# Optimization experiments

Hardware: AMD Instinct MI355X
Metric: run time of the kernel (lower is better)

The kernel has to match this reference:

```python
import jax, jax.numpy as jnp
import numpy as np

N = 50000      # nodes
E = 500000     # edges
R = 4          # num_relations
B = 512        # num graphs in batch
IN = 64        # in_embd
DIN = 6 * IN   # concat of 6 embeddings
H = 256        # layer_embd
O = 256        # out_embd
CARD = [33, 5, 3, 4, 2, 3]


def setup_inputs() -> dict:
    key = jax.random.key(0)
    ks = jax.random.split(key, 24)
    cols = [jax.random.randint(ks[i], (N,), 0, CARD[i], dtype=jnp.int32) for i in range(6)]
    x = jnp.stack(cols, axis=1)                                     # [N,6] categorical atom features
    edge_index = jax.random.randint(ks[6], (2, E), 0, N, dtype=jnp.int32)
    edge_type = jax.random.randint(ks[7], (E,), 0, R, dtype=jnp.int32)
    batch = jnp.sort(jax.random.randint(ks[8], (N,), 0, B, dtype=jnp.int32))

    def g(k, shape, scale):
        return jax.random.normal(k, shape, jnp.float32) * scale

    inp = dict(x=x, edge_index=edge_index, edge_type=edge_type, batch=batch)
    for i in range(6):
        inp[f"emb{i}"] = g(ks[9 + i], (CARD[i], IN), 1.0)
    inp["W1"] = g(ks[15], (R, DIN, H), 0.05)
    inp["root1"] = g(ks[16], (DIN, H), 0.05)
    inp["b1"] = jnp.zeros((H,), jnp.float32)
    inp["W2"] = g(ks[17], (R, H, O), 0.06)
    inp["root2"] = g(ks[18], (H, O), 0.06)
    inp["b2"] = jnp.zeros((O,), jnp.float32)
    inp["g1_w"] = g(ks[19], (O, O), 0.06)
    inp["g1_b"] = jnp.zeros((O,), jnp.float32)
    inp["bn_g"] = jnp.ones((O,), jnp.float32)
    inp["bn_b"] = jnp.zeros((O,), jnp.float32)
    inp["g2_w"] = g(ks[20], (O, 1), 0.06)
    inp["g2_b"] = jnp.zeros((1,), jnp.float32)
    inp["gl_w"] = g(ks[21], (O, 1), 0.06)
    inp["gl_b"] = jnp.zeros((1,), jnp.float32)
    return inp


def rgcn_conv(h, src, dst, etype, W, root, bias):
    # PyG RGCNConv: out_i = x_i @ root + bias + sum_r mean_{j in N_r(i)} (x_j @ W_r)
    xw = jnp.einsum('nd,rdo->rno', h, W)                 # [R,N,O] relation-transformed nodes
    msg = xw[etype, src]                                  # [E,O] gather per edge
    seg = dst * R + etype                                 # combined (node, relation) segment id
    sums = jax.ops.segment_sum(msg, seg, num_segments=N * R)
    cnt = jax.ops.segment_sum(jnp.ones((msg.shape[0],), h.dtype), seg, num_segments=N * R)
    mean = sums / jnp.maximum(cnt, 1.0)[:, None]          # per-relation mean aggregation
    agg = mean.reshape(N, R, -1).sum(axis=1)              # sum over relations
    return agg + h @ root + bias


def reference(x, edge_index, edge_type, batch,
              emb0, emb1, emb2, emb3, emb4, emb5,
              W1, root1, b1, W2, root2, b2,
              g1_w, g1_b, bn_g, bn_b, g2_w, g2_b, gl_w, gl_b):
    embs = [emb0, emb1, emb2, emb3, emb4, emb5]
    feats = jnp.concatenate([embs[i][x[:, i]] for i in range(6)], axis=1)  # [N, 6*IN]
    src, dst = edge_index[0], edge_index[1]
    h = jax.nn.sigmoid(rgcn_conv(feats, src, dst, edge_type, W1, root1, b1))
    h = jax.nn.sigmoid(rgcn_conv(h, src, dst, edge_type, W2, root2, b2))    # [N,O]

    # GlobalAttention gate_nn: Linear -> BatchNorm1d (training-mode stats) -> ReLU -> Linear
    g = h @ g1_w + g1_b
    mu = g.mean(axis=0)
    var = g.var(axis=0)                                   # biased var, as torch BN forward
    g = (g - mu) / jnp.sqrt(var + 1e-5) * bn_g + bn_b
    gate = jax.nn.relu(g) @ g2_w + g2_b                   # [N,1]

    # segment softmax over graphs
    gmax = jax.ops.segment_max(gate, batch, num_segments=B)
    e = jnp.exp(gate - gmax[batch])
    denom = jax.ops.segment_sum(e, batch, num_segments=B)
    attn = e / (denom[batch] + 1e-16)
    pooled = jax.ops.segment_sum(attn * h, batch, num_segments=B)  # [B,O]

    return jax.nn.sigmoid(pooled @ gl_w + gl_b)           # [B,1]
```

## Files before the change

### kernel.cpp

```cpp
#include <hip/hip_runtime.h>
#include <hip/hip_bf16.h>
#include <cstdint>

#define NN 50000
#define NE 500000
#define NR 4
#define NBATCH 512
#define HD 256
#define NSEG (NN*NR)
#define CHUNK 25000

__constant__ int c_off[6] = {0,33,38,41,45,47};

__device__ __forceinline__ float sigf(float x){ return 1.0f/(1.0f+__expf(-x)); }
__device__ __forceinline__ float bf2f(unsigned short b){ return __uint_as_float((unsigned)b<<16); }
__device__ __forceinline__ unsigned short f2bf(float f){
  unsigned u = __float_as_uint(f);
  return (unsigned short)((u + 0x7fffu + ((u>>16)&1u)) >> 16);
}

typedef short bf16raw8 __attribute__((ext_vector_type(8)));
typedef float f32x4v  __attribute__((ext_vector_type(4)));
union LD16 { uint4 u; bf16raw8 v; };

__global__ void k_weff(const float* __restrict__ e0,const float* __restrict__ e1,
                       const float* __restrict__ e2,const float* __restrict__ e3,
                       const float* __restrict__ e4,const float* __restrict__ e5,
                       const float* __restrict__ W, int rstride,
                       float* __restrict__ out){
  int rc = blockIdx.x, h = threadIdx.x;
  int r = rc/50, cg = rc%50;
  int j, cl;
  if      (cg>=47){j=5;cl=cg-47;} else if (cg>=45){j=4;cl=cg-45;}
  else if (cg>=41){j=3;cl=cg-41;} else if (cg>=38){j=2;cl=cg-38;}
  else if (cg>=33){j=1;cl=cg-33;} else            {j=0;cl=cg;}
  const float* emb = j==0?e0:j==1?e1:j==2?e2:j==3?e3:j==4?e4:e5;
  const float* wb = W + (size_t)r*rstride + (size_t)(j*64)*HD + h;
  float acc = 0.f;
  #pragma unroll 8
  for (int k=0;k<64;k++) acc += emb[cl*64+k]*wb[(size_t)k*HD];
  out[(size_t)rc*HD+h] = acc;
}

__global__ void k_cnt(const int* __restrict__ ei, const int* __restrict__ et,
                      int* __restrict__ cnt){
  int e = blockIdx.x*256 + threadIdx.x;
  if (e >= NE) return;
  atomicAdd(&cnt[ei[NE+e]*NR + et[e]], 1);
}

__global__ void k_b1t(const float* __restrict__ W1eff, const float* __restrict__ R1eff,
                      unsigned short* __restrict__ B1t){
  int id = blockIdx.x*256 + threadIdx.x;
  int k = id & 255, o = id >> 8;
  float v = 0.f;
  if (k < 200) v = W1eff[(size_t)k*HD + o];
  else if (k < 250) v = R1eff[(size_t)(k-200)*HD + o];
  B1t[(size_t)o*256 + k] = f2bf(v);
}

__global__ void k_tconv(const float* __restrict__ W, unsigned short* __restrict__ Wt,
                        int K, int O, int dstStride, int dstOff){
  int id = blockIdx.x*256 + threadIdx.x;
  if (id >= K*O) return;
  int k = id % K, o = id / K;
  Wt[(size_t)o*dstStride + dstOff + k] = f2bf(W[(size_t)k*O + o]);
}

#define SC_T 256
#define SC_NB ((NSEG/4 + SC_T - 1)/SC_T)

__global__ void k_scan1(const int* __restrict__ cnt, int* __restrict__ bsum){
  __shared__ int sh[SC_T];
  int b = blockIdx.x, t = threadIdx.x;
  int i4 = b*SC_T + t;
  int s = 0;
  if (i4 < NSEG/4){ int4 v = ((const int4*)cnt)[i4]; s = v.x+v.y+v.z+v.w; }
  sh[t] = s; __syncthreads();
  for (int o=128;o>0;o>>=1){ if (t<o) sh[t]+=sh[t+o]; __syncthreads(); }
  if (t==0) bsum[b] = sh[0];
}

__global__ void k_scan2(const int* __restrict__ bsum, int* __restrict__ boff,
                        int* __restrict__ offs){
  __shared__ int sh[256];
  int t = threadIdx.x;
  int v = (t < SC_NB) ? bsum[t] : 0;
  sh[t] = v; __syncthreads();
  for (int o=1;o<256;o<<=1){
    int add = (t>=o) ? sh[t-o] : 0; __syncthreads();
    sh[t] += add; __syncthreads();
  }
  if (t < SC_NB) boff[t] = sh[t] - v;
  if (t == 255) offs[NSEG] = sh[255];
}

__global__ void k_scan3(const int* __restrict__ cnt, const int* __restrict__ boff,
                        int* __restrict__ offs, int* __restrict__ cursor){
  __shared__ int sh[SC_T];
  int b = blockIdx.x, t = threadIdx.x;
  int i4 = b*SC_T + t;
  int4 v = {0,0,0,0};
  if (i4 < NSEG/4) v = ((const int4*)cnt)[i4];
  int s = v.x+v.y+v.z+v.w;
  sh[t] = s; __syncthreads();
  for (int o=1;o<256;o<<=1){
    int add = (t>=o) ? sh[t-o] : 0; __syncthreads();
    sh[t] += add; __syncthreads();
  }
  if (i4 < NSEG/4){
    int excl = sh[t] - s + boff[b];
    int4 ov; ov.x = excl; ov.y = ov.x+v.x; ov.z = ov.y+v.y; ov.w = ov.z+v.z;
    ((int4*)offs)[i4] = ov; ((int4*)cursor)[i4] = ov;
  }
}

__global__ void k_bin(const int* __restrict__ ei, const int* __restrict__ et,
                      int* __restrict__ cursor, int* __restrict__ esrc){
  int e = blockIdx.x*256 + threadIdx.x;
  if (e >= NE) return;
  int s = ei[e], d = ei[NE+e], t = et[e];
  int slot = atomicAdd(&cursor[d*NR + t], 1);
  esrc[slot] = s;
}

__global__ void k_buildseg(const int* __restrict__ x, const int* __restrict__ offs,
                           const int* __restrict__ esrc, unsigned short* __restrict__ A1){
  int n = blockIdx.x, t = threadIdx.x;
  float v = 0.f;
  if (t < 200){
    int r = t/50, bin = t%50;
    int j, cl;
    if      (bin>=47){j=5;cl=bin-47;} else if (bin>=45){j=4;cl=bin-45;}
    else if (bin>=41){j=3;cl=bin-41;} else if (bin>=38){j=2;cl=bin-38;}
    else if (bin>=33){j=1;cl=bin-33;} else            {j=0;cl=bin;}
    int a = offs[n*NR+r], e2 = offs[n*NR+r+1];
    int c = 0;
    for (int e=a;e<e2;e++){
      int s = esrc[e];
      c += (x[s*6+j] == cl) ? 1 : 0;
    }
    v = (float)c / (float)max(e2-a, 1);
  } else if (t < 250){
    int cg = t - 200;
    #pragma unroll
    for (int j=0;j<6;j++) if (cg == c_off[j] + x[n*6+j]) v = 1.f;
  }
  A1[(size_t)n*256 + t] = f2bf(v);
}

__global__ void k_agg(const int* __restrict__ offs, const int* __restrict__ esrc,
                      const unsigned short* __restrict__ h1, unsigned short* __restrict__ agg,
                      int base, int m){
  int gid = blockIdx.x*256 + threadIdx.x;
  int n = gid >> 6;
  if (n >= m) return;
  int lane = gid & 63;
  int gn = base + n;
  #pragma unroll
  for (int r=0;r<NR;r++){
    int a = offs[gn*NR+r], b = offs[gn*NR+r+1];
    float a0=0.f,a1=0.f,a2=0.f,a3=0.f;
    for (int e=a;e<b;e++){
      int s = esrc[e];
      ushort4 v = *(const ushort4*)(h1 + (size_t)s*HD + lane*4);
      a0+=bf2f(v.x); a1+=bf2f(v.y); a2+=bf2f(v.z); a3+=bf2f(v.w);
    }
    float iv = 1.0f / (float)max(b-a, 1);
    ushort4 o;
    o.x=f2bf(a0*iv); o.y=f2bf(a1*iv); o.z=f2bf(a2*iv); o.w=f2bf(a3*iv);
    *(ushort4*)(agg + (size_t)n*(NR*HD) + r*HD + lane*4) = o;
  }
}

template<int NK1, int NK2, bool SIG>
__global__ __launch_bounds__(512) void k_mfma(
    const unsigned short* __restrict__ A,  int lda,
    const unsigned short* __restrict__ A2, int lda2,
    const unsigned short* __restrict__ Bt,
    const float* __restrict__ bias,
    unsigned short* __restrict__ outB,
    int M){
  constexpr int NK = NK1 + NK2;
  constexpr int K  = NK * 32;
  int tid = threadIdx.x;
  int wave = tid >> 6, lane = tid & 63;
  int wm = (wave >> 1) * 32, wn = (wave & 1) * 64;
  int bm = blockIdx.y * 128, bn = blockIdx.x * 128;
  int lrow = lane & 15, lk8 = (lane >> 4) * 8;

  const unsigned short* aP[2];
  const unsigned short* a2P[2];
  const unsigned short* bP[4];
  #pragma unroll
  for (int mi=0;mi<2;mi++){
    int row = bm + wm + mi*16 + lrow; if (row > M-1) row = M-1;
    aP[mi]  = A  + (size_t)row*lda  + lk8;
    if (NK2 > 0) a2P[mi] = A2 + (size_t)row*lda2 + lk8;
  }
  #pragma unroll
  for (int nj=0;nj<4;nj++){
    int col = bn + wn + nj*16 + lrow;
    bP[nj] = Bt + (size_t)col*K + lk8;
  }

  f32x4v acc[2][4] = {};
  bf16raw8 aF[2][2], bF[2][4];

  #pragma unroll
  for (int mi=0;mi<2;mi++){ LD16 t; t.u = *(const uint4*)(aP[mi]); aF[0][mi]=t.v; }
  #pragma unroll
  for (int nj=0;nj<4;nj++){ LD16 t; t.u = *(const uint4*)(bP[nj]); bF[0][nj]=t.v; }

  #pragma unroll
  for (int k=0;k<NK;k++){
    int cur = k & 1, nxt = cur ^ 1;
    if (k+1 < NK){
      if (k+1 < NK1){
        #pragma unroll
        for (int mi=0;mi<2;mi++){ LD16 t; t.u = *(const uint4*)(aP[mi] + (k+1)*32); aF[nxt][mi]=t.v; }
      } else {
        #pragma unroll
        for (int mi=0;mi<2;mi++){ LD16 t; t.u = *(const uint4*)(a2P[mi] + (k+1-NK1)*32); aF[nxt][mi]=t.v; }
      }
      #pragma unroll
      for (int nj=0;nj<4;nj++){ LD16 t; t.u = *(const uint4*)(bP[nj] + (k+1)*32); bF[nxt][nj]=t.v; }
    }
    #pragma unroll
    for (int mi=0;mi<2;mi++)
      #pragma unroll
      for (int nj=0;nj<4;nj++)
        acc[mi][nj] = __builtin_amdgcn_mfma_f32_16x16x32_bf16(aF[cur][mi], bF[cur][nj], acc[mi][nj], 0, 0, 0);
  }

  int r0 = (lane >> 4) * 4;
  #pragma unroll
  for (int mi = 0; mi < 2; mi++){
    #pragma unroll
    for (int i = 0; i < 4; i++){
      int row = bm + wm + mi*16 + r0 + i;
      if (row >= M) continue;
      #pragma unroll
      for (int nj = 0; nj < 4; nj++){
        int col = bn + wn + nj*16 + lrow;
        float v = acc[mi][nj][i];
        if (bias) v += bias[col];
        if (SIG) v = sigf(v);
        outB[(size_t)row*HD + col] = f2bf(v);
      }
    }
  }
}

__global__ void k_bnstats(const unsigned short* __restrict__ g, float* __restrict__ chan){
  int c = threadIdx.x;
  int r0 = blockIdx.x*128;
  int rend = min(r0+128, NN);
  float s=0.f, q=0.f;
  for (int row=r0; row<rend; row++){
    float v = bf2f(g[(size_t)row*HD + c]);
    s += v; q += v*v;
  }
  atomicAdd(&chan[c], s); atomicAdd(&chan[HD+c], q);
}

__global__ void k_bnfin(const float* __restrict__ chan, const float* __restrict__ bng,
                        const float* __restrict__ bnb, float* __restrict__ bnp){
  int c = threadIdx.x;
  float mu = chan[c]/(float)NN;
  float var = chan[HD+c]/(float)NN - mu*mu;
  float scale = bng[c]*rsqrtf(var + 1e-5f);
  bnp[c] = bnb[c] - mu*scale;
  bnp[HD+c] = scale;
}

__global__ void k_gate(const unsigned short* __restrict__ g, const float* __restrict__ bnp,
                       const float* __restrict__ g2w, const float* __restrict__ g2b,
                       float* __restrict__ gate){
  int lane = threadIdx.x & 63;
  int n = blockIdx.x*4 + (threadIdx.x>>6);
  if (n >= NN) return;
  float s = 0.f;
  #pragma unroll
  for (int k=0;k<4;k++){
    int c = lane + k*64;
    float v = bf2f(g[(size_t)n*HD + c])*bnp[HD+c] + bnp[c];
    v = fmaxf(v, 0.f);
    s += v * g2w[c];
  }
  #pragma unroll
  for (int o=32;o>0;o>>=1) s += __shfl_down(s, o);
  if (lane==0) gate[n] = s + g2b[0];
}

__global__ void k_goffs(const int* __restrict__ batch, int* __restrict__ goffs){
  int n = blockIdx.x*256 + threadIdx.x;
  if (n >= NN) return;
  int b = batch[n];
  int prev = (n == 0) ? -1 : batch[n-1];
  for (int gg = prev+1; gg <= b; gg++) goffs[gg] = n;
  if (n == NN-1){ for (int gg = b+1; gg <= NBATCH; gg++) goffs[gg] = NN; }
}

__global__ __launch_bounds__(256) void k_poolg(
    const unsigned short* __restrict__ h2, const float* __restrict__ gate,
    const int* __restrict__ goffs, const float* __restrict__ glw,
    const float* __restrict__ glb, float* __restrict__ out){
  __shared__ float red[256];
  int b = blockIdx.x, tid = threadIdx.x;
  int a = goffs[b], e = goffs[b+1];

  float m = -3.4e38f;
  for (int n = a + tid; n < e; n += 256) m = fmaxf(m, gate[n]);
  red[tid] = m; __syncthreads();
  for (int o = 128; o > 0; o >>= 1){ if (tid < o) red[tid] = fmaxf(red[tid], red[tid+o]); __syncthreads(); }
  m = red[0]; __syncthreads();

  float s = 0.f;
  for (int n = a + tid; n < e; n += 256) s += __expf(gate[n] - m);
  red[tid] = s; __syncthreads();
  for (int o = 128; o > 0; o >>= 1){ if (tid < o) red[tid] += red[tid+o]; __syncthreads(); }
  float denom = red[0] + 1e-16f; __syncthreads();

  float acc = 0.f;
  #pragma unroll 4
  for (int n = a; n < e; n++){
    float ev = __expf(gate[n] - m);
    acc += ev * bf2f(h2[(size_t)n*HD + tid]);
  }
  acc /= denom;

  red[tid] = acc * glw[tid]; __syncthreads();
  for (int o = 128; o > 0; o >>= 1){ if (tid < o) red[tid] += red[tid+o]; __syncthreads(); }
  if (tid == 0) out[b] = sigf(red[0] + glb[0]);
}

extern "C" void kernel_launch(void* const* d_in, const int* in_sizes, int n_in,
                              void* d_out, int out_size, void* d_ws, size_t ws_size,
                              hipStream_t stream) {
  const int* x     = (const int*)d_in[0];
  const int* ei    = (const int*)d_in[1];
  const int* et    = (const int*)d_in[2];
  const int* batch = (const int*)d_in[3];
  const float* emb0 = (const float*)d_in[4];
  const float* emb1 = (const float*)d_in[5];
  const float* emb2 = (const float*)d_in[6];
  const float* emb3 = (const float*)d_in[7];
  const float* emb4 = (const float*)d_in[8];
  const float* emb5 = (const float*)d_in[9];
  const float* W1    = (const float*)d_in[10];
  const float* root1 = (const float*)d_in[11];
  const float* b1    = (const float*)d_in[12];
  const float* W2    = (const float*)d_in[13];
  const float* root2 = (const float*)d_in[14];
  const float* b2    = (const float*)d_in[15];
  const float* g1w   = (const float*)d_in[16];
  const float* g1b   = (const float*)d_in[17];
  const float* bng   = (const float*)d_in[18];
  const float* bnb   = (const float*)d_in[19];
  const float* g2w   = (const float*)d_in[20];
  const float* g2b   = (const float*)d_in[21];
  const float* glw   = (const float*)d_in[22];
  const float* glb   = (const float*)d_in[23];
  float* out = (float*)d_out;

  char* w = (char*)d_ws;
  auto alloc = [&](size_t bytes)->char* {
    char* p = w; w += (bytes + 255) & ~(size_t)255; return p;
  };
  char* gReg = alloc((size_t)NN*HD*2);
  unsigned short* A1 = (unsigned short*)gReg;
  unsigned short* g  = (unsigned short*)gReg;
  unsigned short* agg  = (unsigned short*)alloc((size_t)CHUNK*NR*HD*2);
  unsigned short* h1   = (unsigned short*)alloc((size_t)NN*HD*2);
  unsigned short* hRes = (unsigned short*)alloc((size_t)NN*HD*2);
  int*   cnt  = (int*)alloc((size_t)NSEG*sizeof(int));
  int*   offs = (int*)alloc((size_t)(NSEG+1)*sizeof(int));
  int*   cursor=(int*)alloc((size_t)NSEG*sizeof(int));
  int*   bsum = (int*)alloc((size_t)SC_NB*sizeof(int));
  int*   boff = (int*)alloc((size_t)SC_NB*sizeof(int));
  int*   esrc = (int*)alloc((size_t)NE*sizeof(int));
  float* W1eff= (float*)alloc((size_t)200*HD*sizeof(float));
  float* R1eff= (float*)alloc((size_t)50*HD*sizeof(float));
  unsigned short* B1t  = (unsigned short*)alloc((size_t)256*256*2);
  unsigned short* BtL2 = (unsigned short*)alloc((size_t)256*1280*2);
  unsigned short* g1wt = (unsigned short*)alloc((size_t)256*256*2);
  float* gate = (float*)alloc((size_t)NN*sizeof(float));
  int*   goffs= (int*)alloc((size_t)(NBATCH+1)*sizeof(int));
  float* chan = (float*)alloc((size_t)2*HD*sizeof(float));
  float* bnp  = (float*)alloc((size_t)2*HD*sizeof(float));

  hipMemsetAsync(cnt,  0, (size_t)NSEG*sizeof(int), stream);
  hipMemsetAsync(chan, 0, (size_t)2*HD*sizeof(float), stream);

  k_weff<<<NR*50, HD, 0, stream>>>(emb0,emb1,emb2,emb3,emb4,emb5, W1, 384*HD, W1eff);
  k_weff<<<50,    HD, 0, stream>>>(emb0,emb1,emb2,emb3,emb4,emb5, root1, 0, R1eff);
  k_b1t<<<256, 256, 0, stream>>>(W1eff, R1eff, B1t);
  k_tconv<<<256, 256, 0, stream>>>(root2, BtL2, 256, 256, 1280, 0);
  k_tconv<<<1024, 256, 0, stream>>>(W2, BtL2, 1024, 256, 1280, 256);
  k_tconv<<<256, 256, 0, stream>>>(g1w, g1wt, 256, 256, 256, 0);

  k_cnt<<<(NE+255)/256, 256, 0, stream>>>(ei, et, cnt);
  k_scan1<<<SC_NB, SC_T, 0, stream>>>(cnt, bsum);
  k_scan2<<<1, 256, 0, stream>>>(bsum, boff, offs);
  k_scan3<<<SC_NB, SC_T, 0, stream>>>(cnt, boff, offs, cursor);
  k_bin<<<(NE+255)/256, 256, 0, stream>>>(ei, et, cursor, esrc);

  k_buildseg<<<NN, 256, 0, stream>>>(x, offs, esrc, A1);

  k_goffs<<<(NN+255)/256, 256, 0, stream>>>(batch, goffs);

  dim3 gFull(2, (NN+127)/128);
  k_mfma<8,0,true><<<gFull, 512, 0, stream>>>(A1, 256, nullptr, 0, B1t, b1, h1, NN);

  for (int c0 = 0; c0 < NN; c0 += CHUNK){
    int m = min(CHUNK, NN - c0);
    k_agg<<<(m*64+255)/256, 256, 0, stream>>>(offs, esrc, h1, agg, c0, m);
    dim3 gC(2, (m+127)/128);
    k_mfma<8,32,true><<<gC, 512, 0, stream>>>(h1 + (size_t)c0*HD, 256, agg, NR*HD,
                                              BtL2, b2, hRes + (size_t)c0*HD, m);
  }

  k_mfma<8,0,false><<<gFull, 512, 0, stream>>>(hRes, 256, nullptr, 0, g1wt, g1b, g, NN);
  k_bnstats<<<(NN+127)/128, HD, 0, stream>>>(g, chan);
  k_bnfin<<<1, HD, 0, stream>>>(chan, bng, bnb, bnp);

  k_gate<<<(NN+3)/4, 256, 0, stream>>>(g, bnp, g2w, g2b, gate);
  k_poolg<<<NBATCH, 256, 0, stream>>>(hRes, gate, goffs, glw, glb, out);
}
```

Measured before the change: 704.5 us.

## Transform-then-aggregate for RGCN layer 2 instead of aggregate-then-GEMM

Layer 2 used to average raw neighbour features per relation into a large K=1280 operand and then run one GEMM. Now it first computes per-relation node transforms h1@W_r (two relations at a time) plus the root term with plain K=256 GEMMs into a z buffer. Two gather kernels then average the transformed rows per relation and finish with bias and sigmoid. This removes the big agg buffer and the chunked loop, at the cost of writing and gathering transformed rows, which adds bf16 rounding of the intermediate terms.

```diff
diff --git a/kernel.cpp b/kernel.cpp
--- a/kernel.cpp
+++ b/kernel.cpp
@@ -8,7 +8,6 @@
 #define NBATCH 512
 #define HD 256
 #define NSEG (NN*NR)
-#define CHUNK 25000
 
 __constant__ int c_off[6] = {0,33,38,41,45,47};
 
@@ -60,11 +59,11 @@
 }
 
 __global__ void k_tconv(const float* __restrict__ W, unsigned short* __restrict__ Wt,
-                        int K, int O, int dstStride, int dstOff){
+                        int K, int O){
   int id = blockIdx.x*256 + threadIdx.x;
   if (id >= K*O) return;
   int k = id % K, o = id / K;
-  Wt[(size_t)o*dstStride + dstOff + k] = f2bf(W[(size_t)k*O + o]);
+  Wt[(size_t)o*256 + k] = f2bf(W[(size_t)k*O + o]);
 }
 
 #define SC_T 256
@@ -149,40 +148,16 @@
   A1[(size_t)n*256 + t] = f2bf(v);
 }
 
-__global__ void k_agg(const int* __restrict__ offs, const int* __restrict__ esrc,
-                      const unsigned short* __restrict__ h1, unsigned short* __restrict__ agg,
-                      int base, int m){
-  int gid = blockIdx.x*256 + threadIdx.x;
-  int n = gid >> 6;
-  if (n >= m) return;
-  int lane = gid & 63;
-  int gn = base + n;
-  #pragma unroll
-  for (int r=0;r<NR;r++){
-    int a = offs[gn*NR+r], b = offs[gn*NR+r+1];
-    float a0=0.f,a1=0.f,a2=0.f,a3=0.f;
-    for (int e=a;e<b;e++){
-      int s = esrc[e];
-      ushort4 v = *(const ushort4*)(h1 + (size_t)s*HD + lane*4);
-      a0+=bf2f(v.x); a1+=bf2f(v.y); a2+=bf2f(v.z); a3+=bf2f(v.w);
-    }
-    float iv = 1.0f / (float)max(b-a, 1);
-    ushort4 o;
-    o.x=f2bf(a0*iv); o.y=f2bf(a1*iv); o.z=f2bf(a2*iv); o.w=f2bf(a3*iv);
-    *(ushort4*)(agg + (size_t)n*(NR*HD) + r*HD + lane*4) = o;
-  }
-}
-
-template<int NK1, int NK2, bool SIG>
+template<bool SIG>
 __global__ __launch_bounds__(512) void k_mfma(
     const unsigned short* __restrict__ A,  int lda,
-    const unsigned short* __restrict__ A2, int lda2,
     const unsigned short* __restrict__ Bt,
     const float* __restrict__ bias,
-    unsigned short* __restrict__ outB,
+    unsigned short* __restrict__ out0, int ldc0, int n0,
+    unsigned short* __restrict__ out1, int ldc1,
     int M){
-  constexpr int NK = NK1 + NK2;
-  constexpr int K  = NK * 32;
+  constexpr int NK = 8;
+  constexpr int K  = 256;
   int tid = threadIdx.x;
   int wave = tid >> 6, lane = tid & 63;
   int wm = (wave >> 1) * 32, wn = (wave & 1) * 64;
@@ -190,13 +165,11 @@
   int lrow = lane & 15, lk8 = (lane >> 4) * 8;
 
   const unsigned short* aP[2];
-  const unsigned short* a2P[2];
   const unsigned short* bP[4];
   #pragma unroll
   for (int mi=0;mi<2;mi++){
     int row = bm + wm + mi*16 + lrow; if (row > M-1) row = M-1;
-    aP[mi]  = A  + (size_t)row*lda  + lk8;
-    if (NK2 > 0) a2P[mi] = A2 + (size_t)row*lda2 + lk8;
+    aP[mi] = A + (size_t)row*lda + lk8;
   }
   #pragma unroll
   for (int nj=0;nj<4;nj++){
@@ -216,13 +189,8 @@
   for (int k=0;k<NK;k++){
     int cur = k & 1, nxt = cur ^ 1;
     if (k+1 < NK){
-      if (k+1 < NK1){
-        #pragma unroll
-        for (int mi=0;mi<2;mi++){ LD16 t; t.u = *(const uint4*)(aP[mi] + (k+1)*32); aF[nxt][mi]=t.v; }
-      } else {
-        #pragma unroll
-        for (int mi=0;mi<2;mi++){ LD16 t; t.u = *(const uint4*)(a2P[mi] + (k+1-NK1)*32); aF[nxt][mi]=t.v; }
-      }
+      #pragma unroll
+      for (int mi=0;mi<2;mi++){ LD16 t; t.u = *(const uint4*)(aP[mi] + (k+1)*32); aF[nxt][mi]=t.v; }
       #pragma unroll
       for (int nj=0;nj<4;nj++){ LD16 t; t.u = *(const uint4*)(bP[nj] + (k+1)*32); bF[nxt][nj]=t.v; }
     }
@@ -246,10 +214,69 @@
         float v = acc[mi][nj][i];
         if (bias) v += bias[col];
         if (SIG) v = sigf(v);
-        outB[(size_t)row*HD + col] = f2bf(v);
+        if (col < n0) out0[(size_t)row*ldc0 + col] = f2bf(v);
+        else          out1[(size_t)row*ldc1 + (col - n0)] = f2bf(v);
       }
     }
   }
+}
+
+__global__ void k_comb1(const int* __restrict__ offs, const int* __restrict__ esrc,
+                        const unsigned short* __restrict__ zbuf,
+                        unsigned short* __restrict__ pacc){
+  int gid = blockIdx.x*256 + threadIdx.x;
+  int n = gid >> 6;
+  if (n >= NN) return;
+  int lane = gid & 63;
+  float t0=0.f,t1=0.f,t2=0.f,t3=0.f;
+  #pragma unroll
+  for (int r=0;r<2;r++){
+    int a = offs[n*NR+r], b = offs[n*NR+r+1];
+    float a0=0.f,a1=0.f,a2=0.f,a3=0.f;
+    for (int e=a;e<b;e++){
+      int s = esrc[e];
+      ushort4 v = *(const ushort4*)(zbuf + (size_t)s*512 + r*256 + lane*4);
+      a0+=bf2f(v.x); a1+=bf2f(v.y); a2+=bf2f(v.z); a3+=bf2f(v.w);
+    }
+    float iv = 1.0f / (float)max(b-a, 1);
+    t0+=a0*iv; t1+=a1*iv; t2+=a2*iv; t3+=a3*iv;
+  }
+  ushort4 o; o.x=f2bf(t0); o.y=f2bf(t1); o.z=f2bf(t2); o.w=f2bf(t3);
+  *(ushort4*)(pacc + (size_t)n*HD + lane*4) = o;
+}
+
+__global__ void k_comb2(const int* __restrict__ offs, const int* __restrict__ esrc,
+                        const unsigned short* __restrict__ zbuf,
+                        const unsigned short* __restrict__ pacc,
+                        const unsigned short* __restrict__ rootbuf,
+                        const float* __restrict__ b2,
+                        unsigned short* __restrict__ h2){
+  int gid = blockIdx.x*256 + threadIdx.x;
+  int n = gid >> 6;
+  if (n >= NN) return;
+  int lane = gid & 63;
+  float t0=0.f,t1=0.f,t2=0.f,t3=0.f;
+  #pragma unroll
+  for (int r=0;r<2;r++){
+    int a = offs[n*NR+2+r], b = offs[n*NR+2+r+1];
+    float a0=0.f,a1=0.f,a2=0.f,a3=0.f;
+    for (int e=a;e<b;e++){
+      int s = esrc[e];
+      ushort4 v = *(const ushort4*)(zbuf + (size_t)s*512 + r*256 + lane*4);
+      a0+=bf2f(v.x); a1+=bf2f(v.y); a2+=bf2f(v.z); a3+=bf2f(v.w);
+    }
+    float iv = 1.0f / (float)max(b-a, 1);
+    t0+=a0*iv; t1+=a1*iv; t2+=a2*iv; t3+=a3*iv;
+  }
+  ushort4 p = *(const ushort4*)(pacc + (size_t)n*HD + lane*4);
+  ushort4 rt= *(const ushort4*)(rootbuf + (size_t)n*HD + lane*4);
+  float4 bb = *(const float4*)(b2 + lane*4);
+  ushort4 o;
+  o.x = f2bf(sigf(t0 + bf2f(p.x) + bf2f(rt.x) + bb.x));
+  o.y = f2bf(sigf(t1 + bf2f(p.y) + bf2f(rt.y) + bb.y));
+  o.z = f2bf(sigf(t2 + bf2f(p.z) + bf2f(rt.z) + bb.z));
+  o.w = f2bf(sigf(t3 + bf2f(p.w) + bf2f(rt.w) + bb.w));
+  *(ushort4*)(h2 + (size_t)n*HD + lane*4) = o;
 }
 
 __global__ void k_bnstats(const unsigned short* __restrict__ g, float* __restrict__ chan){
@@ -368,22 +395,25 @@
   auto alloc = [&](size_t bytes)->char* {
     char* p = w; w += (bytes + 255) & ~(size_t)255; return p;
   };
-  char* gReg = alloc((size_t)NN*HD*2);
-  unsigned short* A1 = (unsigned short*)gReg;
-  unsigned short* g  = (unsigned short*)gReg;
-  unsigned short* agg  = (unsigned short*)alloc((size_t)CHUNK*NR*HD*2);
-  unsigned short* h1   = (unsigned short*)alloc((size_t)NN*HD*2);
-  unsigned short* hRes = (unsigned short*)alloc((size_t)NN*HD*2);
+  char* slotA = alloc((size_t)NN*HD*2);
+  unsigned short* A1      = (unsigned short*)slotA;
+  unsigned short* rootbuf = (unsigned short*)slotA;
+  unsigned short* g       = (unsigned short*)slotA;
+  unsigned short* h1 = (unsigned short*)alloc((size_t)NN*HD*2);
+  unsigned short* h2 = h1;
+  unsigned short* zbuf = (unsigned short*)alloc((size_t)NN*512*2);
+  unsigned short* pacc = (unsigned short*)alloc((size_t)NN*HD*2);
   int*   cnt  = (int*)alloc((size_t)NSEG*sizeof(int));
+  int*   cursor = cnt;
   int*   offs = (int*)alloc((size_t)(NSEG+1)*sizeof(int));
-  int*   cursor=(int*)alloc((size_t)NSEG*sizeof(int));
   int*   bsum = (int*)alloc((size_t)SC_NB*sizeof(int));
   int*   boff = (int*)alloc((size_t)SC_NB*sizeof(int));
   int*   esrc = (int*)alloc((size_t)NE*sizeof(int));
   float* W1eff= (float*)alloc((size_t)200*HD*sizeof(float));
   float* R1eff= (float*)alloc((size_t)50*HD*sizeof(float));
   unsigned short* B1t  = (unsigned short*)alloc((size_t)256*256*2);
-  unsigned short* BtL2 = (unsigned short*)alloc((size_t)256*1280*2);
+  unsigned short* Btz1 = (unsigned short*)alloc((size_t)768*256*2);
+  unsigned short* Btz2 = (unsigned short*)alloc((size_t)512*256*2);
   unsigned short* g1wt = (unsigned short*)alloc((size_t)256*256*2);
   float* gate = (float*)alloc((size_t)NN*sizeof(float));
   int*   goffs= (int*)alloc((size_t)(NBATCH+1)*sizeof(int));
@@ -396,9 +426,12 @@
   k_weff<<<NR*50, HD, 0, stream>>>(emb0,emb1,emb2,emb3,emb4,emb5, W1, 384*HD, W1eff);
   k_weff<<<50,    HD, 0, stream>>>(emb0,emb1,emb2,emb3,emb4,emb5, root1, 0, R1eff);
   k_b1t<<<256, 256, 0, stream>>>(W1eff, R1eff, B1t);
-  k_tconv<<<256, 256, 0, stream>>>(root2, BtL2, 256, 256, 1280, 0);
-  k_tconv<<<1024, 256, 0, stream>>>(W2, BtL2, 1024, 256, 1280, 256);
-  k_tconv<<<256, 256, 0, stream>>>(g1w, g1wt, 256, 256, 256, 0);
+  k_tconv<<<256, 256, 0, stream>>>(W2,               Btz1,           256, 256);
+  k_tconv<<<256, 256, 0, stream>>>(W2 + 256*256,     Btz1 + 256*256, 256, 256);
+  k_tconv<<<256, 256, 0, stream>>>(root2,            Btz1 + 512*256, 256, 256);
+  k_tconv<<<256, 256, 0, stream>>>(W2 + 2*256*256,   Btz2,           256, 256);
+  k_tconv<<<256, 256, 0, stream>>>(W2 + 3*256*256,   Btz2 + 256*256, 256, 256);
+  k_tconv<<<256, 256, 0, stream>>>(g1w,              g1wt,           256, 256);
 
   k_cnt<<<(NE+255)/256, 256, 0, stream>>>(ei, et, cnt);
   k_scan1<<<SC_NB, SC_T, 0, stream>>>(cnt, bsum);
@@ -410,21 +443,21 @@
 
   k_goffs<<<(NN+255)/256, 256, 0, stream>>>(batch, goffs);
 
-  dim3 gFull(2, (NN+127)/128);
-  k_mfma<8,0,true><<<gFull, 512, 0, stream>>>(A1, 256, nullptr, 0, B1t, b1, h1, NN);
-
-  for (int c0 = 0; c0 < NN; c0 += CHUNK){
-    int m = min(CHUNK, NN - c0);
-    k_agg<<<(m*64+255)/256, 256, 0, stream>>>(offs, esrc, h1, agg, c0, m);
-    dim3 gC(2, (m+127)/128);
-    k_mfma<8,32,true><<<gC, 512, 0, stream>>>(h1 + (size_t)c0*HD, 256, agg, NR*HD,
-                                              BtL2, b2, hRes + (size_t)c0*HD, m);
-  }
-
-  k_mfma<8,0,false><<<gFull, 512, 0, stream>>>(hRes, 256, nullptr, 0, g1wt, g1b, g, NN);
+  dim3 g256(2, (NN+127)/128);
+  k_mfma<true><<<g256, 512, 0, stream>>>(A1, 256, B1t, b1, h1, 256, 256, nullptr, 0, NN);
+
+  dim3 g768(6, (NN+127)/128);
+  k_mfma<false><<<g768, 512, 0, stream>>>(h1, 256, Btz1, nullptr, zbuf, 512, 512, rootbuf, 256, NN);
+  k_comb1<<<(NN*64+255)/256, 256, 0, stream>>>(offs, esrc, zbuf, pacc);
+
+  dim3 g512(4, (NN+127)/128);
+  k_mfma<false><<<g512, 512, 0, stream>>>(h1, 256, Btz2, nullptr, zbuf, 512, 512, nullptr, 0, NN);
+  k_comb2<<<(NN*64+255)/256, 256, 0, stream>>>(offs, esrc, zbuf, pacc, rootbuf, b2, h2);
+
+  k_mfma<false><<<g256, 512, 0, stream>>>(h2, 256, g1wt, g1b, g, 256, 256, nullptr, 0, NN);
   k_bnstats<<<(NN+127)/128, HD, 0, stream>>>(g, chan);
   k_bnfin<<<1, HD, 0, stream>>>(chan, bng, bnb, bnp);
 
   k_gate<<<(NN+3)/4, 256, 0, stream>>>(g, bnp, g2w, g2b, gate);
-  k_poolg<<<NBATCH, 256, 0, stream>>>(hRes, gate, goffs, glw, glb, out);
-}
+  k_poolg<<<NBATCH, 256, 0, stream>>>(h2, gate, goffs, glw, glb, out);
+}
```

Result: faster. 688.3 us (-2.3%).
